# Kernel optimization log

Measured on AMD Instinct MI355X. Metric: run time of the kernel, lower is better.

## Reference

```python
import jax, jax.numpy as jnp
import numpy as np

H = 1024  # hidden_size
B = 32
S = 1024


def setup_inputs() -> dict:
    key = jax.random.key(0)
    ks = jax.random.split(key, 8)
    sc_e = 1.0 / np.sqrt(2 * H)
    sc_d = 1.0 / np.sqrt(H)
    return {
        "context": jax.random.normal(ks[0], (B, S, 2 * H), dtype=jnp.float32),
        "dec_hidden": jax.random.normal(ks[1], (B, H), dtype=jnp.float32),
        # linear_encoder: 2H -> H
        "We": jax.random.uniform(ks[2], (2 * H, H), jnp.float32, -sc_e, sc_e),
        "be": jax.random.uniform(ks[3], (H,), jnp.float32, -sc_e, sc_e),
        # linear_decoder: H -> H
        "Wd": jax.random.uniform(ks[4], (H, H), jnp.float32, -sc_d, sc_d),
        "bd": jax.random.uniform(ks[5], (H,), jnp.float32, -sc_d, sc_d),
        # linear_v: H -> 1
        "Wv": jax.random.uniform(ks[6], (H, 1), jnp.float32, -sc_d, sc_d),
        "bv": jax.random.uniform(ks[7], (1,), jnp.float32, -sc_d, sc_d),
    }


def reference(context, dec_hidden, We, be, Wd, bd, Wv, bv):
    # gamma_encoder: [B, S, H]
    gamma_enc = jnp.einsum("bse,eh->bsh", context, We) + be
    # gamma_decoder: [B, 1, H]
    gamma_dec = (dec_hidden @ Wd + bd)[:, None, :]
    # scores: [B, S]
    scores = jnp.tanh(gamma_enc + gamma_dec) @ Wv  # [B, S, 1]
    scores = scores[..., 0] + bv[0]
    weights = jax.nn.softmax(scores, axis=1)  # [B, S]
    # c_t: [B, 2H]
    c_t = jnp.einsum("bs,bse->be", weights, context)
    return (c_t, weights)
```

## Files before the change

kernel.cpp:

```cpp
#include <hip/hip_runtime.h>
#include <hip/hip_bf16.h>

typedef __attribute__((ext_vector_type(4))) float  f32x4;
typedef __attribute__((ext_vector_type(8))) short  short8;

#define H_    1024
#define K_    2048
#define B_    32
#define S_    1024
#define M_TOT 32768

static __device__ __forceinline__ unsigned short f2bf(float f) {
  __hip_bfloat16 h = __float2bfloat16(f);
  return __builtin_bit_cast(unsigned short, h);
}
static __device__ __forceinline__ float bf2f(unsigned short u) {
  unsigned int x = ((unsigned int)u) << 16;
  return __builtin_bit_cast(float, x);
}

static __device__ __forceinline__ float fast_tanh(float x) {
  float e = __builtin_amdgcn_exp2f(x * 2.88539008177792681f);
  return 1.0f - 2.0f * __builtin_amdgcn_rcpf(e + 1.0f);
}

static __device__ __forceinline__ void gload_lds16(const void* g, void* l) {
  __builtin_amdgcn_global_load_lds(
      (const __attribute__((address_space(1))) unsigned int*)g,
      (__attribute__((address_space(3))) unsigned int*)l, 16, 0, 0);
}

__global__ __launch_bounds__(256)
void ctx_convert_kernel(const float* __restrict__ ctx,
                        unsigned short* __restrict__ ctxb) {
  int idx = blockIdx.x * 256 + threadIdx.x;
#pragma unroll
  for (int j = 0; j < 16; ++j) {
    size_t e = ((size_t)j * 524288 + idx) * 8;
    f32x4 a = *(const f32x4*)(ctx + e);
    f32x4 b = *(const f32x4*)(ctx + e + 4);
    short8 v;
    v[0] = (short)f2bf(a[0]); v[1] = (short)f2bf(a[1]);
    v[2] = (short)f2bf(a[2]); v[3] = (short)f2bf(a[3]);
    v[4] = (short)f2bf(b[0]); v[5] = (short)f2bf(b[1]);
    v[6] = (short)f2bf(b[2]); v[7] = (short)f2bf(b[3]);
    *(short8*)(ctxb + e) = v;
  }
}

__global__ void we_transpose_kernel(const float* __restrict__ We,
                                    unsigned short* __restrict__ WeT) {
  __shared__ float tile[32][33];
  int k0 = blockIdx.x * 32;
  int n0 = blockIdx.y * 32;
  int tx = threadIdx.x, ty = threadIdx.y;
#pragma unroll
  for (int i = 0; i < 32; i += 8)
    tile[ty + i][tx] = We[(size_t)(k0 + ty + i) * H_ + n0 + tx];
  __syncthreads();
#pragma unroll
  for (int i = 0; i < 32; i += 8)
    WeT[(size_t)(n0 + ty + i) * K_ + k0 + tx] = f2bf(tile[tx][ty + i]);
}

__global__ void gdec_kernel(const float* __restrict__ dec,
                            const float* __restrict__ Wd,
                            const float* __restrict__ bd,
                            float* __restrict__ gdec) {
  int h = blockIdx.x * 256 + threadIdx.x;
  int b = blockIdx.y;
  const float* dp = dec + b * H_;
  float acc = bd[h];
#pragma unroll 8
  for (int k = 0; k < H_; ++k) acc += dp[k] * Wd[(size_t)k * H_ + h];
  gdec[b * H_ + h] = acc;
}

__global__ __launch_bounds__(512, 2)
void gemm_score_kernel(const unsigned short* __restrict__ Abf,
                       const unsigned short* __restrict__ WeT,
                       const float* __restrict__ be,
                       const float* __restrict__ gdec,
                       const float* __restrict__ Wv,
                       float* __restrict__ spart_g) {
  __shared__ __align__(16) unsigned short As[4][256 * 32];
  __shared__ __align__(16) unsigned short Bs[4][256 * 32];
  __shared__ float bg[256];
  __shared__ float wvl[256];
  __shared__ float sred[4][256];

  const int tid  = threadIdx.x;
  const int lane = tid & 63;
  const int wid  = tid >> 6;
  const int wr   = wid >> 2;
  const int wc   = wid & 3;
  const int lc = lane & 15, l4 = lane >> 4;

  const int bid = blockIdx.x;
  const int x   = bid & 7;
  const int c   = bid >> 3;
  const int mt  = x * 16 + (c >> 2);
  const int nt  = c & 3;
  const int m0  = mt * 256;
  const int n0  = nt * 256;
  const int b   = m0 >> 10;

  if (tid < 256) {
    bg[tid]  = be[n0 + tid] + gdec[b * H_ + n0 + tid];
    wvl[tid] = Wv[n0 + tid];
  }

  const int srow = lane >> 2;
  const int csw  = ((lane & 3) ^ (srow & 3)) * 8;
  const unsigned short* aB = Abf + (size_t)(m0 + wid * 16 + srow) * K_ + csw;
  const unsigned short* bB = WeT + (size_t)(n0 + wid * 16 + srow) * K_ + csw;

  f32x4 acc[8][4];
#pragma unroll
  for (int mi = 0; mi < 8; ++mi)
#pragma unroll
    for (int ni = 0; ni < 4; ++ni) {
      f32x4 z = {0.f, 0.f, 0.f, 0.f};
      acc[mi][ni] = z;
    }

  auto STAGE = [&](int bi, int j) {
    const int ko = j * 32;
#pragma unroll
    for (int i = 0; i < 2; ++i) {
      gload_lds16(aB + (size_t)i * 128 * K_ + ko,
                  &As[bi][(i * 128 + wid * 16) * 32]);
      gload_lds16(bB + (size_t)i * 128 * K_ + ko,
                  &Bs[bi][(i * 128 + wid * 16) * 32]);
    }
  };
  auto COMPUTE = [&](int bi) {
    short8 bfr[4];
#pragma unroll
    for (int ni = 0; ni < 4; ++ni) {
      int r = wc * 64 + ni * 16 + lc;
      bfr[ni] = *(const short8*)((const char*)&Bs[bi][0] + r * 64 +
                                 ((l4 ^ (lc & 3)) << 4));
    }
#pragma unroll
    for (int mh = 0; mh < 2; ++mh) {
      short8 afr[4];
#pragma unroll
      for (int mi = 0; mi < 4; ++mi) {
        int r = wr * 128 + mh * 64 + mi * 16 + lc;
        afr[mi] = *(const short8*)((const char*)&As[bi][0] + r * 64 +
                                   ((l4 ^ (lc & 3)) << 4));
      }
      __builtin_amdgcn_s_setprio(1);
#pragma unroll
      for (int mi = 0; mi < 4; ++mi)
#pragma unroll
        for (int ni = 0; ni < 4; ++ni)
          acc[mh * 4 + mi][ni] = __builtin_amdgcn_mfma_f32_16x16x32_bf16(
              afr[mi], bfr[ni], acc[mh * 4 + mi][ni], 0, 0, 0);
      __builtin_amdgcn_s_setprio(0);
    }
  };

#define GS_ITER(j, bi)                                    \
  do {                                                    \
    COMPUTE(bi);                                          \
    STAGE(((bi) + 2) & 3, (j) + 2);                       \
    asm volatile("s_waitcnt vmcnt(4)" ::: "memory");      \
    __builtin_amdgcn_s_barrier();                         \
    __builtin_amdgcn_sched_barrier(0);                    \
  } while (0)

  STAGE(0, 0);
  STAGE(1, 1);
  asm volatile("s_waitcnt vmcnt(4) lgkmcnt(0)" ::: "memory");
  __builtin_amdgcn_s_barrier();
  __builtin_amdgcn_sched_barrier(0);

  for (int jj = 0; jj < 60; jj += 4) {
    GS_ITER(jj + 0, 0);
    GS_ITER(jj + 1, 1);
    GS_ITER(jj + 2, 2);
    GS_ITER(jj + 3, 3);
  }
  GS_ITER(60, 0);
  GS_ITER(61, 1);
  COMPUTE(2);
  asm volatile("s_waitcnt vmcnt(0)" ::: "memory");
  __builtin_amdgcn_s_barrier();
  __builtin_amdgcn_sched_barrier(0);
  COMPUTE(3);
#undef GS_ITER

#pragma unroll
  for (int ami = 0; ami < 8; ++ami) {
#pragma unroll
    for (int j = 0; j < 4; ++j) {
      float s = 0.f;
#pragma unroll
      for (int ni = 0; ni < 4; ++ni) {
        int cC  = wc * 64 + ni * 16 + lc;
        s += fast_tanh(acc[ami][ni][j] + bg[cC]) * wvl[cC];
      }
#pragma unroll
      for (int off = 1; off < 16; off <<= 1) s += __shfl_xor(s, off);
      if (lc == 0) sred[wc][wr * 128 + ami * 16 + l4 * 4 + j] = s;
    }
  }
  __syncthreads();
  if (tid < 256)
    spart_g[(size_t)nt * M_TOT + m0 + tid] =
        sred[0][tid] + sred[1][tid] + sred[2][tid] + sred[3][tid];
}

__global__ void softmax_kernel(const float* __restrict__ spart,
                               const float* __restrict__ bv,
                               float* __restrict__ wout, int nparts) {
  int b = blockIdx.x, tid = threadIdx.x;
  int lane = tid & 63, wid = tid >> 6;
  __shared__ float red[4];
  float bv0 = bv[0];
  float v[4];
#pragma unroll
  for (int i = 0; i < 4; ++i) {
    int m = b * S_ + i * 256 + tid;
    float s = bv0;
    for (int nb = 0; nb < nparts; ++nb) s += spart[(size_t)nb * M_TOT + m];
    v[i] = s;
  }
  float mx = fmaxf(fmaxf(v[0], v[1]), fmaxf(v[2], v[3]));
#pragma unroll
  for (int off = 1; off < 64; off <<= 1) mx = fmaxf(mx, __shfl_xor(mx, off));
  if (lane == 0) red[wid] = mx;
  __syncthreads();
  mx = fmaxf(fmaxf(red[0], red[1]), fmaxf(red[2], red[3]));
  __syncthreads();
  float e[4], sum = 0.f;
#pragma unroll
  for (int i = 0; i < 4; ++i) {
    e[i] = expf(v[i] - mx);
    sum += e[i];
  }
#pragma unroll
  for (int off = 1; off < 64; off <<= 1) sum += __shfl_xor(sum, off);
  if (lane == 0) red[wid] = sum;
  __syncthreads();
  sum = red[0] + red[1] + red[2] + red[3];
  float inv = 1.f / sum;
#pragma unroll
  for (int i = 0; i < 4; ++i)
    wout[b * S_ + i * 256 + tid] = e[i] * inv;
}

__global__ __launch_bounds__(256)
void ct_partial_bf_kernel(const unsigned short* __restrict__ ctxb,
                          const float* __restrict__ w,
                          float* __restrict__ part) {
  int tid = threadIdx.x;
  int b = blockIdx.x, sc = blockIdx.y;
  int e0 = tid * 8;
  const float* wp = w + b * S_ + sc * 32;
  const unsigned short* cp = ctxb + (size_t)(b * S_ + sc * 32) * K_ + e0;
  float acc[8];
#pragma unroll
  for (int j = 0; j < 8; ++j) acc[j] = 0.f;
#pragma unroll 4
  for (int s = 0; s < 32; ++s) {
    float ws_ = wp[s];
    short8 v = *(const short8*)(cp + (size_t)s * K_);
#pragma unroll
    for (int j = 0; j < 8; ++j)
      acc[j] += ws_ * bf2f((unsigned short)v[j]);
  }
  float* dst = part + (size_t)sc * 65536 + (size_t)b * K_ + e0;
#pragma unroll
  for (int j = 0; j < 8; ++j) dst[j] = acc[j];
}

__global__ void ct_combine32_kernel(const float* __restrict__ part,
                                    float* __restrict__ out) {
  int idx = blockIdx.x * 256 + threadIdx.x;
  float s = 0.f;
#pragma unroll
  for (int p = 0; p < 32; ++p) s += part[(size_t)p * 65536 + idx];
  out[idx] = s;
}

extern "C" void kernel_launch(void* const* d_in, const int* in_sizes, int n_in,
                              void* d_out, int out_size, void* d_ws, size_t ws_size,
                              hipStream_t stream) {
  const float* ctx = (const float*)d_in[0];
  const float* dec = (const float*)d_in[1];
  const float* We  = (const float*)d_in[2];
  const float* be  = (const float*)d_in[3];
  const float* Wd  = (const float*)d_in[4];
  const float* bd  = (const float*)d_in[5];
  const float* Wv  = (const float*)d_in[6];
  const float* bv  = (const float*)d_in[7];
  float* out = (float*)d_out;
  char*  ws  = (char*)d_ws;

  const size_t SZ_ABF  = (size_t)M_TOT * K_ * 2;
  const size_t OFF_WET = SZ_ABF;
  const size_t OFF_GD  = OFF_WET + (size_t)H_ * K_ * 2;
  const size_t OFF_SP  = OFF_GD + (size_t)B_ * H_ * 4;
  const size_t OFF_CT  = OFF_SP + (size_t)8 * M_TOT * 4;

  unsigned short* Abf  = (unsigned short*)ws;
  unsigned short* WeT  = (unsigned short*)(ws + OFF_WET);
  float*          gdec = (float*)(ws + OFF_GD);
  float*          spart= (float*)(ws + OFF_SP);
  float*          ctpt = (float*)(ws + OFF_CT);

  ctx_convert_kernel<<<2048, 256, 0, stream>>>(ctx, Abf);
  we_transpose_kernel<<<dim3(K_ / 32, H_ / 32), dim3(32, 8), 0, stream>>>(We, WeT);
  gdec_kernel<<<dim3(H_ / 256, B_), 256, 0, stream>>>(dec, Wd, bd, gdec);
  gemm_score_kernel<<<512, 512, 0, stream>>>(Abf, WeT, be, gdec, Wv, spart);
  softmax_kernel<<<B_, 256, 0, stream>>>(spart, bv, out + 65536, 4);
  ct_partial_bf_kernel<<<dim3(B_, 32), 256, 0, stream>>>(Abf, out + 65536, ctpt);
  ct_combine32_kernel<<<256, 256, 0, stream>>>(ctpt, out);
}
```

Before: 309.1 us.

## Restructure GEMM main loop into double-buffered 64-wide K tiles with interleaved staging

```diff
diff --git a/kernel.cpp b/kernel.cpp
--- a/kernel.cpp
+++ b/kernel.cpp
@@ -76,15 +76,15 @@
   gdec[b * H_ + h] = acc;
 }
 
-__global__ __launch_bounds__(512, 2)
+__global__ __launch_bounds__(512)
 void gemm_score_kernel(const unsigned short* __restrict__ Abf,
                        const unsigned short* __restrict__ WeT,
                        const float* __restrict__ be,
                        const float* __restrict__ gdec,
                        const float* __restrict__ Wv,
                        float* __restrict__ spart_g) {
-  __shared__ __align__(16) unsigned short As[4][256 * 32];
-  __shared__ __align__(16) unsigned short Bs[4][256 * 32];
+  __shared__ __align__(16) unsigned short As[2][2][256 * 32];
+  __shared__ __align__(16) unsigned short Bs[2][2][256 * 32];
   __shared__ float bg[256];
   __shared__ float wvl[256];
   __shared__ float sred[4][256];
@@ -98,9 +98,9 @@
 
   const int bid = blockIdx.x;
   const int x   = bid & 7;
-  const int c   = bid >> 3;
-  const int mt  = x * 16 + (c >> 2);
-  const int nt  = c & 3;
+  const int c_  = bid >> 3;
+  const int mt  = x * 16 + (c_ >> 2);
+  const int nt  = c_ & 3;
   const int m0  = mt * 256;
   const int n0  = nt * 256;
   const int b   = m0 >> 10;
@@ -111,9 +111,12 @@
   }
 
   const int srow = lane >> 2;
-  const int csw  = ((lane & 3) ^ (srow & 3)) * 8;
+  const int skey = (srow & 3) ^ ((srow >> 2) & 3);
+  const int csw  = ((lane & 3) ^ skey) * 8;
   const unsigned short* aB = Abf + (size_t)(m0 + wid * 16 + srow) * K_ + csw;
   const unsigned short* bB = WeT + (size_t)(n0 + wid * 16 + srow) * K_ + csw;
+
+  const int rdsw = ((l4 ^ ((lc & 3) ^ ((lc >> 2) & 3))) << 4);
 
   f32x4 acc[8][4];
 #pragma unroll
@@ -124,73 +127,96 @@
       acc[mi][ni] = z;
     }
 
-  auto STAGE = [&](int bi, int j) {
-    const int ko = j * 32;
-#pragma unroll
-    for (int i = 0; i < 2; ++i) {
-      gload_lds16(aB + (size_t)i * 128 * K_ + ko,
-                  &As[bi][(i * 128 + wid * 16) * 32]);
-      gload_lds16(bB + (size_t)i * 128 * K_ + ko,
-                  &Bs[bi][(i * 128 + wid * 16) * 32]);
-    }
-  };
-  auto COMPUTE = [&](int bi) {
-    short8 bfr[4];
-#pragma unroll
-    for (int ni = 0; ni < 4; ++ni) {
-      int r = wc * 64 + ni * 16 + lc;
-      bfr[ni] = *(const short8*)((const char*)&Bs[bi][0] + r * 64 +
-                                 ((l4 ^ (lc & 3)) << 4));
-    }
-#pragma unroll
-    for (int mh = 0; mh < 2; ++mh) {
-      short8 afr[4];
-#pragma unroll
-      for (int mi = 0; mi < 4; ++mi) {
-        int r = wr * 128 + mh * 64 + mi * 16 + lc;
-        afr[mi] = *(const short8*)((const char*)&As[bi][0] + r * 64 +
-                                   ((l4 ^ (lc & 3)) << 4));
-      }
-      __builtin_amdgcn_s_setprio(1);
-#pragma unroll
-      for (int mi = 0; mi < 4; ++mi)
-#pragma unroll
-        for (int ni = 0; ni < 4; ++ni)
-          acc[mh * 4 + mi][ni] = __builtin_amdgcn_mfma_f32_16x16x32_bf16(
-              afr[mi], bfr[ni], acc[mh * 4 + mi][ni], 0, 0, 0);
-      __builtin_amdgcn_s_setprio(0);
-    }
-  };
-
-#define GS_ITER(j, bi)                                    \
-  do {                                                    \
-    COMPUTE(bi);                                          \
-    STAGE(((bi) + 2) & 3, (j) + 2);                       \
-    asm volatile("s_waitcnt vmcnt(4)" ::: "memory");      \
-    __builtin_amdgcn_s_barrier();                         \
-    __builtin_amdgcn_sched_barrier(0);                    \
-  } while (0)
-
-  STAGE(0, 0);
-  STAGE(1, 1);
-  asm volatile("s_waitcnt vmcnt(4) lgkmcnt(0)" ::: "memory");
-  __builtin_amdgcn_s_barrier();
+  short8 afr[4], bfr[4];
+
+#define STAGE_A(bb, kh, tn)                                                  \
+  do {                                                                       \
+    const int koA = (tn) * 64 + (kh) * 32;                                   \
+    gload_lds16(aB + koA, &As[bb][kh][(wid * 16) * 32]);                     \
+    gload_lds16(aB + (size_t)128 * K_ + koA,                                 \
+                &As[bb][kh][(128 + wid * 16) * 32]);                         \
+  } while (0)
+#define STAGE_B(bb, kh, tn)                                                  \
+  do {                                                                       \
+    const int koB = (tn) * 64 + (kh) * 32;                                   \
+    gload_lds16(bB + koB, &Bs[bb][kh][(wid * 16) * 32]);                     \
+    gload_lds16(bB + (size_t)128 * K_ + koB,                                 \
+                &Bs[bb][kh][(128 + wid * 16) * 32]);                         \
+  } while (0)
+#define READ_B(cc, ks)                                                       \
+  do {                                                                       \
+    _Pragma("unroll") for (int ni = 0; ni < 4; ++ni) {                       \
+      int r = wc * 64 + ni * 16 + lc;                                        \
+      bfr[ni] = *(const short8*)((const char*)&Bs[cc][ks][0] + r * 64 + rdsw);\
+    }                                                                        \
+  } while (0)
+#define READ_A(cc, ks, mh)                                                   \
+  do {                                                                       \
+    _Pragma("unroll") for (int mi = 0; mi < 4; ++mi) {                       \
+      int r = wr * 128 + (mh) * 64 + mi * 16 + lc;                           \
+      afr[mi] = *(const short8*)((const char*)&As[cc][ks][0] + r * 64 + rdsw);\
+    }                                                                        \
+  } while (0)
+#define MFMA16(mh)                                                           \
+  do {                                                                       \
+    __builtin_amdgcn_s_setprio(1);                                           \
+    _Pragma("unroll") for (int mi = 0; mi < 4; ++mi)                         \
+      _Pragma("unroll") for (int ni = 0; ni < 4; ++ni)                       \
+        acc[(mh) * 4 + mi][ni] = __builtin_amdgcn_mfma_f32_16x16x32_bf16(    \
+            afr[mi], bfr[ni], acc[(mh) * 4 + mi][ni], 0, 0, 0);              \
+    __builtin_amdgcn_s_setprio(0);                                           \
+  } while (0)
+#define LGKM0                                                                \
+  asm volatile("s_waitcnt lgkmcnt(0)" ::: "memory");                         \
+  __builtin_amdgcn_sched_barrier(0)
+#define VM4 asm volatile("s_waitcnt vmcnt(4)" ::: "memory")
+#define BAR __builtin_amdgcn_s_barrier()
+
+#define TILE(t, cc)                                                          \
+  do {                                                                       \
+    const int tn = ((t) + 1) & 31;                                           \
+                                                    \
+    READ_B(cc, 0); READ_A(cc, 0, 0);                                         \
+    STAGE_A(cc ^ 1, 0, tn);                                                  \
+    BAR; LGKM0; MFMA16(0); BAR;                                              \
+                                                    \
+    READ_A(cc, 0, 1);                                                        \
+    STAGE_B(cc ^ 1, 0, tn);                                                  \
+    BAR; LGKM0; MFMA16(1);                                                   \
+    VM4; BAR;                       \
+                                                    \
+    READ_B(cc, 1); READ_A(cc, 1, 0);                                         \
+    STAGE_A(cc ^ 1, 1, tn);                                                  \
+    BAR; LGKM0; MFMA16(0); BAR;                                              \
+                                                    \
+    READ_A(cc, 1, 1);                                                        \
+    STAGE_B(cc ^ 1, 1, tn);                                                  \
+    BAR; LGKM0; MFMA16(1);                                                   \
+    VM4; BAR;              \
+  } while (0)
+
+  STAGE_A(0, 0, 0);
+  STAGE_B(0, 0, 0);
+  STAGE_A(0, 1, 0);
+  STAGE_B(0, 1, 0);
+  VM4;
+  BAR;
   __builtin_amdgcn_sched_barrier(0);
 
-  for (int jj = 0; jj < 60; jj += 4) {
-    GS_ITER(jj + 0, 0);
-    GS_ITER(jj + 1, 1);
-    GS_ITER(jj + 2, 2);
-    GS_ITER(jj + 3, 3);
-  }
-  GS_ITER(60, 0);
-  GS_ITER(61, 1);
-  COMPUTE(2);
-  asm volatile("s_waitcnt vmcnt(0)" ::: "memory");
-  __builtin_amdgcn_s_barrier();
-  __builtin_amdgcn_sched_barrier(0);
-  COMPUTE(3);
-#undef GS_ITER
+  for (int tp = 0; tp < 16; ++tp) {
+    TILE(2 * tp, 0);
+    TILE(2 * tp + 1, 1);
+  }
+
+#undef TILE
+#undef STAGE_A
+#undef STAGE_B
+#undef READ_A
+#undef READ_B
+#undef MFMA16
+#undef LGKM0
+#undef VM4
+#undef BAR
 
 #pragma unroll
   for (int ami = 0; ami < 8; ++ami) {
```

Measured after the change: 330.4 us. 6.9% more time.

## Load We fragments directly from global into registers and stage only A in LDS

Applied to the files above, without the earlier changes.

```diff
diff --git a/kernel.cpp b/kernel.cpp
--- a/kernel.cpp
+++ b/kernel.cpp
@@ -76,15 +76,14 @@
   gdec[b * H_ + h] = acc;
 }
 
-__global__ __launch_bounds__(512, 2)
+__global__ __launch_bounds__(512)
 void gemm_score_kernel(const unsigned short* __restrict__ Abf,
                        const unsigned short* __restrict__ WeT,
                        const float* __restrict__ be,
                        const float* __restrict__ gdec,
                        const float* __restrict__ Wv,
                        float* __restrict__ spart_g) {
-  __shared__ __align__(16) unsigned short As[4][256 * 32];
-  __shared__ __align__(16) unsigned short Bs[4][256 * 32];
+  __shared__ __align__(16) unsigned short As[2][256 * 64];
   __shared__ float bg[256];
   __shared__ float wvl[256];
   __shared__ float sred[4][256];
@@ -110,10 +109,22 @@
     wvl[tid] = Wv[n0 + tid];
   }
 
-  const int srow = lane >> 2;
-  const int csw  = ((lane & 3) ^ (srow & 3)) * 8;
-  const unsigned short* aB = Abf + (size_t)(m0 + wid * 16 + srow) * K_ + csw;
-  const unsigned short* bB = WeT + (size_t)(n0 + wid * 16 + srow) * K_ + csw;
+  const int g8  = lane >> 3;
+  const int csw = ((lane & 7) ^ g8) * 8;
+  const unsigned short* aB = Abf + (size_t)(m0 + wid * 8 + g8) * K_ + csw;
+
+  const unsigned short* bD = WeT + (size_t)(n0 + wc * 64 + lc) * K_ + l4 * 8;
+
+  int aoff[2][8];
+#pragma unroll
+  for (int ks = 0; ks < 2; ++ks)
+#pragma unroll
+    for (int mh = 0; mh < 2; ++mh)
+#pragma unroll
+      for (int mi = 0; mi < 4; ++mi) {
+        int r = wr * 128 + mh * 64 + mi * 16 + lc;
+        aoff[ks][mh * 4 + mi] = r * 128 + ((((ks << 2) | l4) ^ (lc & 7)) << 4);
+      }
 
   f32x4 acc[8][4];
 #pragma unroll
@@ -124,33 +135,26 @@
       acc[mi][ni] = z;
     }
 
-  auto STAGE = [&](int bi, int j) {
-    const int ko = j * 32;
-#pragma unroll
-    for (int i = 0; i < 2; ++i) {
-      gload_lds16(aB + (size_t)i * 128 * K_ + ko,
-                  &As[bi][(i * 128 + wid * 16) * 32]);
-      gload_lds16(bB + (size_t)i * 128 * K_ + ko,
-                  &Bs[bi][(i * 128 + wid * 16) * 32]);
-    }
+  short8 bfr0[4], bfr1[4];
+
+  auto ASTAGE = [&](int bi, int tn) {
+    const int ko = tn * 64;
+#pragma unroll
+    for (int g = 0; g < 4; ++g)
+      gload_lds16(aB + (size_t)g * 64 * K_ + ko, &As[bi][(g * 64 + wid * 8) * 64]);
   };
-  auto COMPUTE = [&](int bi) {
-    short8 bfr[4];
-#pragma unroll
-    for (int ni = 0; ni < 4; ++ni) {
-      int r = wc * 64 + ni * 16 + lc;
-      bfr[ni] = *(const short8*)((const char*)&Bs[bi][0] + r * 64 +
-                                 ((l4 ^ (lc & 3)) << 4));
-    }
+  auto BLOAD = [&](short8* dst, int tn, int ks) {
+#pragma unroll
+    for (int ni = 0; ni < 4; ++ni)
+      dst[ni] = *(const short8*)(bD + (size_t)ni * 16 * K_ + tn * 64 + ks * 32);
+  };
+  auto COMPUTE_KS = [&](int bi, int ks, const short8* bfr) {
 #pragma unroll
     for (int mh = 0; mh < 2; ++mh) {
       short8 afr[4];
 #pragma unroll
-      for (int mi = 0; mi < 4; ++mi) {
-        int r = wr * 128 + mh * 64 + mi * 16 + lc;
-        afr[mi] = *(const short8*)((const char*)&As[bi][0] + r * 64 +
-                                   ((l4 ^ (lc & 3)) << 4));
-      }
+      for (int mi = 0; mi < 4; ++mi)
+        afr[mi] = *(const short8*)((const char*)&As[bi][0] + aoff[ks][mh * 4 + mi]);
       __builtin_amdgcn_s_setprio(1);
 #pragma unroll
       for (int mi = 0; mi < 4; ++mi)
@@ -162,35 +166,28 @@
     }
   };
 
-#define GS_ITER(j, bi)                                    \
-  do {                                                    \
-    COMPUTE(bi);                                          \
-    STAGE(((bi) + 2) & 3, (j) + 2);                       \
-    asm volatile("s_waitcnt vmcnt(4)" ::: "memory");      \
-    __builtin_amdgcn_s_barrier();                         \
-    __builtin_amdgcn_sched_barrier(0);                    \
-  } while (0)
-
-  STAGE(0, 0);
-  STAGE(1, 1);
-  asm volatile("s_waitcnt vmcnt(4) lgkmcnt(0)" ::: "memory");
-  __builtin_amdgcn_s_barrier();
-  __builtin_amdgcn_sched_barrier(0);
-
-  for (int jj = 0; jj < 60; jj += 4) {
-    GS_ITER(jj + 0, 0);
-    GS_ITER(jj + 1, 1);
-    GS_ITER(jj + 2, 2);
-    GS_ITER(jj + 3, 3);
-  }
-  GS_ITER(60, 0);
-  GS_ITER(61, 1);
-  COMPUTE(2);
+  ASTAGE(0, 0);
+  BLOAD(bfr0, 0, 0);
   asm volatile("s_waitcnt vmcnt(0)" ::: "memory");
   __builtin_amdgcn_s_barrier();
   __builtin_amdgcn_sched_barrier(0);
-  COMPUTE(3);
-#undef GS_ITER
+
+#pragma unroll 2
+  for (int kt = 0; kt < 32; ++kt) {
+    const int cur = kt & 1;
+    if (kt < 31) ASTAGE(cur ^ 1, kt + 1);
+    BLOAD(bfr1, kt, 1);
+    COMPUTE_KS(cur, 0, bfr0);
+    if (kt < 31) BLOAD(bfr0, kt + 1, 0);
+    COMPUTE_KS(cur, 1, bfr1);
+    if (kt < 31) {
+      asm volatile("s_waitcnt vmcnt(4)" ::: "memory");
+    } else {
+      asm volatile("s_waitcnt vmcnt(0)" ::: "memory");
+    }
+    __builtin_amdgcn_s_barrier();
+    __builtin_amdgcn_sched_barrier(0);
+  }
 
 #pragma unroll
   for (int ami = 0; ami < 8; ++ami) {
```

New measurement: 350.6 us. 13.4% more time.
